# Optimization experiments

Measured on AMD Instinct MI355X. Metric: run time of the kernel, lower is better.

The kernel has to match this reference:

```python
import jax, jax.numpy as jnp
import numpy as np

B, A, T, D = 8, 50, 256, 128
HEADS, C = 32, 4  # C = D // HEADS
NEG_SLOPE = 0.2   # PyG GATConv default negative_slope


def setup_inputs() -> dict:
    key = jax.random.key(0)
    k1, k2, k3, k4 = jax.random.split(key, 4)
    h = jax.random.normal(k1, (B, A, T, D), dtype=jnp.float32)
    # PyG Linear weight [heads*out, in], applied as x @ W.T
    W = jax.random.normal(k2, (HEADS * C, D), dtype=jnp.float32) * (1.0 / np.sqrt(D))
    att_src = jax.random.normal(k3, (HEADS, C), dtype=jnp.float32) * 0.1
    att_dst = jax.random.normal(k4, (HEADS, C), dtype=jnp.float32) * 0.1
    bias = jnp.zeros((HEADS * C,), dtype=jnp.float32)
    return {"h": h, "W": W, "att_src": att_src, "att_dst": att_dst, "bias": bias}


def reference(h, W, att_src, att_dst, bias):
    # Graph is fully-connected-minus-self over A agents, replicated B*T times.
    # Equivalent dense form: per-destination softmax over all sources j != i.
    Bv, Av, Tv, Dv = h.shape
    x = h.transpose(0, 2, 1, 3).reshape(Bv * Tv, Av, Dv)          # [N, A, D], N = B*T graphs
    x = jnp.einsum('nad,ed->nae', x, W).reshape(Bv * Tv, Av, HEADS, C)  # W x, per head
    a_src = jnp.einsum('nahc,hc->nah', x, att_src)                # alpha_src[j]
    a_dst = jnp.einsum('nahc,hc->nah', x, att_dst)                # alpha_dst[i]
    # edge (j -> i): e_ij = leaky_relu(alpha_src[j] + alpha_dst[i])
    e = a_dst[:, :, None, :] + a_src[:, None, :, :]               # [N, i, j, H]
    e = jnp.where(e > 0, e, NEG_SLOPE * e)
    diag = jnp.eye(Av, dtype=bool)[None, :, :, None]              # no self-loops
    e = jnp.where(diag, -jnp.inf, e)
    alpha = jax.nn.softmax(e, axis=2)                             # scatter-softmax over src per dst
    out = jnp.einsum('nijh,njhc->nihc', alpha, x)                 # scatter-add aggregation
    out = out.reshape(Bv * Tv, Av, HEADS * C) + bias              # concat heads + bias
    return out.reshape(Bv, Tv, Av, HEADS * C).transpose(0, 2, 1, 3)  # (B, A, T, D)
```

## Files before the change

kernel.cpp:

```cpp
#include <hip/hip_runtime.h>
#include <hip/hip_bf16.h>

#define LOG2E 1.4426950408889634f

typedef __attribute__((ext_vector_type(8))) short bf16x8;
typedef __attribute__((ext_vector_type(4))) float f32x4;
typedef __attribute__((ext_vector_type(2))) float v2f;

static __device__ __forceinline__ float fast_exp2(float x) {
    return __builtin_amdgcn_exp2f(x);
}
static __device__ __forceinline__ short bf16bits(float f) {
    __hip_bfloat16 b = __float2bfloat16(f);
    return *reinterpret_cast<short*>(&b);
}
static __device__ __forceinline__ float bfbits2f(unsigned lo16) {
    return __uint_as_float(lo16 << 16);
}

__global__ void wconv(const float* __restrict__ W, short* __restrict__ Wb) {
    const int i = blockIdx.x * 256 + threadIdx.x;
    Wb[i] = bf16bits(W[i]);
}

template<bool PRE>
__global__ __launch_bounds__(256, 4) void gat_fused(
    const float* __restrict__ hsrc,
    const float* __restrict__ W,
    const short* __restrict__ Wb,
    const float* __restrict__ att_src,
    const float* __restrict__ att_dst,
    const float* __restrict__ bias,
    float* __restrict__ out)
{
    constexpr int A = 50, T = 256, D = 128, H = 32;
    __shared__ __align__(16) char smem[52 * 32 * 16 + A * H * 8];
    char*  cxs  = smem;
    v2f*   EdFd = (v2f*)(smem + 26624);
    short* hsb  = (short*)smem;

    const int n = blockIdx.x;
    const int b = n >> 8;
    const int t = n & 255;
    const int tid = threadIdx.x;
    const int lane = tid & 63, lr = lane & 15, lg = lane >> 4;
    const int wv = tid >> 6;

    const float4* hg4 = (const float4*)hsrc;
    for (int idx = tid; idx < 64 * 32; idx += 256) {
        const int a = idx >> 5, k4 = idx & 31;
        short4 pk = {0, 0, 0, 0};
        if (a < A) {
            const float4 hv = hg4[((size_t)(b * A + a) * T + t) * 32 + k4];
            pk.x = bf16bits(hv.x); pk.y = bf16bits(hv.y);
            pk.z = bf16bits(hv.z); pk.w = bf16bits(hv.w);
        }
        const int swz = (k4 >> 1) ^ (a & 7);
        *(short4*)&hsb[a * 128 + swz * 8 + (k4 & 1) * 4] = pk;
    }
    __syncthreads();

    {
        const int n0 = wv * 32;
        f32x4 acc[4][2];
        #pragma unroll
        for (int m = 0; m < 4; ++m) {
            acc[m][0] = (f32x4){0.f, 0.f, 0.f, 0.f};
            acc[m][1] = (f32x4){0.f, 0.f, 0.f, 0.f};
        }
        #pragma unroll
        for (int kk = 0; kk < 4; ++kk) {
            bf16x8 bf0, bf1;
            if (PRE) {
                const bf16x8* Wb8 = (const bf16x8*)Wb;
                bf0 = Wb8[(size_t)(n0 + lr) * 16 + kk * 4 + lg];
                bf1 = Wb8[(size_t)(n0 + 16 + lr) * 16 + kk * 4 + lg];
            } else {
                const float4* W4 = (const float4*)W;
                const int kb = kk * 8 + lg * 2;
                const float4 wa = W4[(size_t)(n0 + lr) * 32 + kb];
                const float4 wb = W4[(size_t)(n0 + lr) * 32 + kb + 1];
                const float4 wc = W4[(size_t)(n0 + 16 + lr) * 32 + kb];
                const float4 wd = W4[(size_t)(n0 + 16 + lr) * 32 + kb + 1];
                bf0[0] = bf16bits(wa.x); bf0[1] = bf16bits(wa.y);
                bf0[2] = bf16bits(wa.z); bf0[3] = bf16bits(wa.w);
                bf0[4] = bf16bits(wb.x); bf0[5] = bf16bits(wb.y);
                bf0[6] = bf16bits(wb.z); bf0[7] = bf16bits(wb.w);
                bf1[0] = bf16bits(wc.x); bf1[1] = bf16bits(wc.y);
                bf1[2] = bf16bits(wc.z); bf1[3] = bf16bits(wc.w);
                bf1[4] = bf16bits(wd.x); bf1[5] = bf16bits(wd.y);
                bf1[6] = bf16bits(wd.z); bf1[7] = bf16bits(wd.w);
            }
            #pragma unroll
            for (int m = 0; m < 4; ++m) {
                const int row = m * 16 + lr;
                const int chunk = (kk * 4 + lg) ^ (row & 7);
                const bf16x8 af = *(const bf16x8*)&hsb[row * 128 + chunk * 8];
                acc[m][0] = __builtin_amdgcn_mfma_f32_16x16x32_bf16(af, bf0, acc[m][0], 0, 0, 0);
                acc[m][1] = __builtin_amdgcn_mfma_f32_16x16x32_bf16(af, bf1, acc[m][1], 0, 0, 0);
            }
        }
        __syncthreads();
        #pragma unroll
        for (int m = 0; m < 4; ++m) {
            #pragma unroll
            for (int nt = 0; nt < 2; ++nt) {
                const int col = n0 + nt * 16 + lr;
                const int boff = (col >> 2) * 16 + (col & 3) * 2;
                #pragma unroll
                for (int r = 0; r < 4; ++r) {
                    const int row = m * 16 + lg * 4 + r;
                    if (row < 52)
                        *(short*)&cxs[row * 512 + boff] = bf16bits(acc[m][nt][r]);
                }
            }
        }
    }
    __syncthreads();

    for (int idx = tid; idx < A * H; idx += 256) {
        const int hh = idx & 31;
        const uint2 xq = *(const uint2*)&cxs[idx * 16];
        const float x0 = bfbits2f(xq.x & 0xffffu);
        const float x1 = __uint_as_float(xq.x & 0xffff0000u);
        const float x2 = bfbits2f(xq.y & 0xffffu);
        const float x3 = __uint_as_float(xq.y & 0xffff0000u);
        const float4 s4 = ((const float4*)att_src)[hh];
        const float4 d4 = ((const float4*)att_dst)[hh];
        const float asc = LOG2E * fmaf(x3, s4.w, fmaf(x2, s4.z, fmaf(x1, s4.y, x0 * s4.x)));
        const float ads = LOG2E * fmaf(x3, d4.w, fmaf(x2, d4.z, fmaf(x1, d4.y, x0 * d4.x)));
        *(v2f*)&cxs[idx * 16 + 8] = (v2f){fast_exp2(asc), fast_exp2(0.2f * asc)};
        EdFd[idx] = (v2f){fast_exp2(ads), fast_exp2(0.2f * ads)};
    }
    __syncthreads();

    {
        const int hh = tid & 31;
        const int ib = tid >> 5;
        v2f acc01[7], acc23[7], df[7];
        float l[7];
        #pragma unroll
        for (int r = 0; r < 7; ++r) {
            const int i = ib + 8 * r;
            const int ii = (i < A) ? i : (A - 1);
            df[r] = EdFd[ii * H + hh];
            acc01[r] = (v2f){0.f, 0.f};
            acc23[r] = (v2f){0.f, 0.f};
            l[r] = 0.f;
        }
        const char* cp = &cxs[hh * 16];
        uint4 cur = *(const uint4*)cp;
        #pragma unroll 2
        for (int j = 0; j < A; ++j) {
            const uint4 nxt = *(const uint4*)(cp + (j + 1) * 512);
            const v2f sf = (v2f){__uint_as_float(cur.z), __uint_as_float(cur.w)};
            const v2f x01 = (v2f){bfbits2f(cur.x & 0xffffu),
                                  __uint_as_float(cur.x & 0xffff0000u)};
            const v2f x23 = (v2f){bfbits2f(cur.y & 0xffffu),
                                  __uint_as_float(cur.y & 0xffff0000u)};
            #pragma unroll
            for (int r = 0; r < 7; ++r) {
                const v2f pe = df[r] * sf;
                const float p = fmaxf(pe.x, pe.y);
                l[r] += p;
                const v2f pp = (v2f){p, p};
                acc01[r] = __builtin_elementwise_fma(pp, x01, acc01[r]);
                acc23[r] = __builtin_elementwise_fma(pp, x23, acc23[r]);
            }
            cur = nxt;
        }
        const float4 bv = ((const float4*)bias)[hh];
        #pragma unroll
        for (int r = 0; r < 7; ++r) {
            const int i = ib + 8 * r;
            if (i < A) {
                const uint4 ce = *(const uint4*)&cxs[(i * 32 + hh) * 16];
                const v2f sf = (v2f){__uint_as_float(ce.z), __uint_as_float(ce.w)};
                const float xx0 = bfbits2f(ce.x & 0xffffu);
                const float xx1 = __uint_as_float(ce.x & 0xffff0000u);
                const float xx2 = bfbits2f(ce.y & 0xffffu);
                const float xx3 = __uint_as_float(ce.y & 0xffff0000u);
                const v2f pe = df[r] * sf;
                const float p = fmaxf(pe.x, pe.y);
                const float linv = 1.0f / (l[r] - p);
                float4 o;
                o.x = fmaf(acc01[r].x - p * xx0, linv, bv.x);
                o.y = fmaf(acc01[r].y - p * xx1, linv, bv.y);
                o.z = fmaf(acc23[r].x - p * xx2, linv, bv.z);
                o.w = fmaf(acc23[r].y - p * xx3, linv, bv.w);
                *(float4*)&out[((size_t)(b * A + i) * T + t) * D + hh * 4] = o;
            }
        }
    }
}

extern "C" void kernel_launch(void* const* d_in, const int* in_sizes, int n_in,
                              void* d_out, int out_size, void* d_ws, size_t ws_size,
                              hipStream_t stream) {
    const float* h       = (const float*)d_in[0];
    const float* W       = (const float*)d_in[1];
    const float* att_src = (const float*)d_in[2];
    const float* att_dst = (const float*)d_in[3];
    const float* bias    = (const float*)d_in[4];
    float* out = (float*)d_out;
    dim3 grid(8 * 256);
    dim3 block(256);
    if (ws_size >= 128 * 128 * sizeof(short)) {
        short* Wb = (short*)d_ws;
        hipLaunchKernelGGL(wconv, dim3(64), block, 0, stream, W, Wb);
        hipLaunchKernelGGL(gat_fused<true>, grid, block, 0, stream,
                           h, W, Wb, att_src, att_dst, bias, out);
    } else {
        hipLaunchKernelGGL(gat_fused<false>, grid, block, 0, stream,
                           h, W, (const short*)nullptr, att_src, att_dst, bias, out);
    }
}
```

Before: 59.54 us.

## Split fused GAT kernel into coalesced bf16 projection GEMM and attention pass

Splits the fused kernel into two kernels. A GEMM kernel reads h in contiguous 64-timestep tiles per agent, projects it with MFMA and writes a bf16 intermediate laid out per graph. A separate attention kernel then reads that compact intermediate per (b,t) graph. The aim is to replace the strided gather of h, where each graph touches 50 scattered rows, with coalesced reads. The cost is an extra launch plus a write and read of a bf16 intermediate of about 26MB through global memory.

```diff
diff --git a/kernel.cpp b/kernel.cpp
--- a/kernel.cpp
+++ b/kernel.cpp
@@ -17,10 +17,194 @@
 static __device__ __forceinline__ float bfbits2f(unsigned lo16) {
     return __uint_as_float(lo16 << 16);
 }
+static __device__ __forceinline__ unsigned packbf(float lo, float hi) {
+    return (unsigned)(unsigned short)bf16bits(lo)
+         | ((unsigned)(unsigned short)bf16bits(hi) << 16);
+}
 
 __global__ void wconv(const float* __restrict__ W, short* __restrict__ Wb) {
     const int i = blockIdx.x * 256 + threadIdx.x;
     Wb[i] = bf16bits(W[i]);
+}
+
+__global__ __launch_bounds__(256, 2) void xgemm(
+    const float* __restrict__ hsrc,
+    const short* __restrict__ Wb,
+    short* __restrict__ Xg)
+{
+    __shared__ __align__(16) char smem[64 * 136 * 4];
+    short* hsb  = (short*)smem;
+    float* xout = (float*)smem;
+
+    const int beta = blockIdx.x;
+    const int b   = beta / 200;
+    const int rem = beta % 200;
+    const int a   = rem >> 2;
+    const int tb  = rem & 3;
+    const int tid = threadIdx.x;
+    const int lane = tid & 63, lr = lane & 15, lg = lane >> 4;
+    const int wv = tid >> 6;
+
+    const float4* hg4 = (const float4*)(hsrc + (((size_t)(b * 50 + a) * 256) + tb * 64) * 128);
+    for (int idx = tid; idx < 64 * 32; idx += 256) {
+        const int u = idx >> 5, k4 = idx & 31;
+        const float4 hv = hg4[u * 32 + k4];
+        short4 pk;
+        pk.x = bf16bits(hv.x); pk.y = bf16bits(hv.y);
+        pk.z = bf16bits(hv.z); pk.w = bf16bits(hv.w);
+        const int swz = (k4 >> 1) ^ (u & 7);
+        *(short4*)&hsb[u * 128 + swz * 8 + (k4 & 1) * 4] = pk;
+    }
+    __syncthreads();
+
+    const int n0 = wv * 32;
+    f32x4 acc[4][2];
+    #pragma unroll
+    for (int m = 0; m < 4; ++m) {
+        acc[m][0] = (f32x4){0.f, 0.f, 0.f, 0.f};
+        acc[m][1] = (f32x4){0.f, 0.f, 0.f, 0.f};
+    }
+    const bf16x8* Wb8 = (const bf16x8*)Wb;
+    #pragma unroll
+    for (int kk = 0; kk < 4; ++kk) {
+        const bf16x8 bf0 = Wb8[(size_t)(n0 + lr) * 16 + kk * 4 + lg];
+        const bf16x8 bf1 = Wb8[(size_t)(n0 + 16 + lr) * 16 + kk * 4 + lg];
+        #pragma unroll
+        for (int m = 0; m < 4; ++m) {
+            const int row = m * 16 + lr;
+            const int chunk = (kk * 4 + lg) ^ (row & 7);
+            const bf16x8 af = *(const bf16x8*)&hsb[row * 128 + chunk * 8];
+            acc[m][0] = __builtin_amdgcn_mfma_f32_16x16x32_bf16(af, bf0, acc[m][0], 0, 0, 0);
+            acc[m][1] = __builtin_amdgcn_mfma_f32_16x16x32_bf16(af, bf1, acc[m][1], 0, 0, 0);
+        }
+    }
+    __syncthreads();
+
+    #pragma unroll
+    for (int m = 0; m < 4; ++m) {
+        #pragma unroll
+        for (int nt = 0; nt < 2; ++nt) {
+            const int col = n0 + nt * 16 + lr;
+            #pragma unroll
+            for (int r = 0; r < 4; ++r) {
+                xout[(m * 16 + lg * 4 + r) * 136 + col] = acc[m][nt][r];
+            }
+        }
+    }
+    __syncthreads();
+
+    short* base = Xg + (((size_t)b * 256 + tb * 64) * 50 + (size_t)a) * 128;
+    for (int idx = tid; idx < 1024; idx += 256) {
+        const int u = idx >> 4, seg = idx & 15;
+        const float4 f0 = *(const float4*)&xout[u * 136 + seg * 8];
+        const float4 f1 = *(const float4*)&xout[u * 136 + seg * 8 + 4];
+        uint4 o;
+        o.x = packbf(f0.x, f0.y); o.y = packbf(f0.z, f0.w);
+        o.z = packbf(f1.x, f1.y); o.w = packbf(f1.z, f1.w);
+        *(uint4*)&base[(size_t)u * 6400 + seg * 8] = o;
+    }
+}
+
+__global__ __launch_bounds__(256, 4) void gat_attn(
+    const short* __restrict__ Xg,
+    const float* __restrict__ att_src,
+    const float* __restrict__ att_dst,
+    const float* __restrict__ bias,
+    float* __restrict__ out)
+{
+    constexpr int A = 50, T = 256, D = 128, H = 32;
+    __shared__ __align__(16) char smem[52 * 32 * 16 + A * H * 8];
+    char* cxs  = smem;
+    v2f*  EdFd = (v2f*)(smem + 26624);
+
+    const int n = blockIdx.x;
+    const int b = n >> 8;
+    const int t = n & 255;
+    const int tid = threadIdx.x;
+
+    const short* xb = Xg + (size_t)n * 6400;
+    for (int idx = tid; idx < 52 * 32; idx += 256) {
+        uint2 v = {0u, 0u};
+        if (idx < A * H) v = *(const uint2*)&xb[idx * 4];
+        *(uint2*)&cxs[idx * 16] = v;
+        *(v2f*)&cxs[idx * 16 + 8] = (v2f){0.f, 0.f};
+    }
+    __syncthreads();
+
+    for (int idx = tid; idx < A * H; idx += 256) {
+        const int hh = idx & 31;
+        const uint2 xq = *(const uint2*)&cxs[idx * 16];
+        const float x0 = bfbits2f(xq.x & 0xffffu);
+        const float x1 = __uint_as_float(xq.x & 0xffff0000u);
+        const float x2 = bfbits2f(xq.y & 0xffffu);
+        const float x3 = __uint_as_float(xq.y & 0xffff0000u);
+        const float4 s4 = ((const float4*)att_src)[hh];
+        const float4 d4 = ((const float4*)att_dst)[hh];
+        const float asc = LOG2E * fmaf(x3, s4.w, fmaf(x2, s4.z, fmaf(x1, s4.y, x0 * s4.x)));
+        const float ads = LOG2E * fmaf(x3, d4.w, fmaf(x2, d4.z, fmaf(x1, d4.y, x0 * d4.x)));
+        *(v2f*)&cxs[idx * 16 + 8] = (v2f){fast_exp2(asc), fast_exp2(0.2f * asc)};
+        EdFd[idx] = (v2f){fast_exp2(ads), fast_exp2(0.2f * ads)};
+    }
+    __syncthreads();
+
+    {
+        const int hh = tid & 31;
+        const int ib = tid >> 5;
+        v2f acc01[7], acc23[7], df[7];
+        float l[7];
+        #pragma unroll
+        for (int r = 0; r < 7; ++r) {
+            const int i = ib + 8 * r;
+            const int ii = (i < A) ? i : (A - 1);
+            df[r] = EdFd[ii * H + hh];
+            acc01[r] = (v2f){0.f, 0.f};
+            acc23[r] = (v2f){0.f, 0.f};
+            l[r] = 0.f;
+        }
+        const char* cp = &cxs[hh * 16];
+        uint4 cur = *(const uint4*)cp;
+        #pragma unroll 2
+        for (int j = 0; j < A; ++j) {
+            const uint4 nxt = *(const uint4*)(cp + (j + 1) * 512);
+            const v2f sf = (v2f){__uint_as_float(cur.z), __uint_as_float(cur.w)};
+            const v2f x01 = (v2f){bfbits2f(cur.x & 0xffffu),
+                                  __uint_as_float(cur.x & 0xffff0000u)};
+            const v2f x23 = (v2f){bfbits2f(cur.y & 0xffffu),
+                                  __uint_as_float(cur.y & 0xffff0000u)};
+            #pragma unroll
+            for (int r = 0; r < 7; ++r) {
+                const v2f pe = df[r] * sf;
+                const float p = fmaxf(pe.x, pe.y);
+                l[r] += p;
+                const v2f pp = (v2f){p, p};
+                acc01[r] = __builtin_elementwise_fma(pp, x01, acc01[r]);
+                acc23[r] = __builtin_elementwise_fma(pp, x23, acc23[r]);
+            }
+            cur = nxt;
+        }
+        const float4 bv = ((const float4*)bias)[hh];
+        #pragma unroll
+        for (int r = 0; r < 7; ++r) {
+            const int i = ib + 8 * r;
+            if (i < A) {
+                const uint4 ce = *(const uint4*)&cxs[(i * 32 + hh) * 16];
+                const v2f sf = (v2f){__uint_as_float(ce.z), __uint_as_float(ce.w)};
+                const float xx0 = bfbits2f(ce.x & 0xffffu);
+                const float xx1 = __uint_as_float(ce.x & 0xffff0000u);
+                const float xx2 = bfbits2f(ce.y & 0xffffu);
+                const float xx3 = __uint_as_float(ce.y & 0xffff0000u);
+                const v2f pe = df[r] * sf;
+                const float p = fmaxf(pe.x, pe.y);
+                const float linv = 1.0f / (l[r] - p);
+                float4 o;
+                o.x = fmaf(acc01[r].x - p * xx0, linv, bv.x);
+                o.y = fmaf(acc01[r].y - p * xx1, linv, bv.y);
+                o.z = fmaf(acc23[r].x - p * xx2, linv, bv.z);
+                o.w = fmaf(acc23[r].y - p * xx3, linv, bv.w);
+                *(float4*)&out[((size_t)(b * A + i) * T + t) * D + hh * 4] = o;
+            }
+        }
+    }
 }
 
 template<bool PRE>
@@ -203,15 +387,25 @@
     const float* att_dst = (const float*)d_in[3];
     const float* bias    = (const float*)d_in[4];
     float* out = (float*)d_out;
-    dim3 grid(8 * 256);
     dim3 block(256);
-    if (ws_size >= 128 * 128 * sizeof(short)) {
+
+    const size_t needW = 128 * 128 * sizeof(short);
+    const size_t needX = (size_t)2048 * 50 * 128 * sizeof(short);
+
+    if (ws_size >= needW + needX) {
+        short* Wb = (short*)d_ws;
+        short* Xg = (short*)((char*)d_ws + needW);
+        hipLaunchKernelGGL(wconv, dim3(64), block, 0, stream, W, Wb);
+        hipLaunchKernelGGL(xgemm, dim3(1600), block, 0, stream, h, Wb, Xg);
+        hipLaunchKernelGGL(gat_attn, dim3(2048), block, 0, stream,
+                           Xg, att_src, att_dst, bias, out);
+    } else if (ws_size >= needW) {
         short* Wb = (short*)d_ws;
         hipLaunchKernelGGL(wconv, dim3(64), block, 0, stream, W, Wb);
-        hipLaunchKernelGGL(gat_fused<true>, grid, block, 0, stream,
+        hipLaunchKernelGGL(gat_fused<true>, dim3(2048), block, 0, stream,
                            h, W, Wb, att_src, att_dst, bias, out);
     } else {
-        hipLaunchKernelGGL(gat_fused<false>, grid, block, 0, stream,
+        hipLaunchKernelGGL(gat_fused<false>, dim3(2048), block, 0, stream,
                            h, W, (const short*)nullptr, att_src, att_dst, bias, out);
     }
 }
```

Result: slower. 71.59 us (+20.2%).
